# Performance work log

Measured on AMD Instinct MI355X. Metric: run time of the kernel, lower is better.

Reference implementation:

```python
import jax, jax.numpy as jnp
import numpy as np

D = 1024
H = 16
HD = D // H
MLP = 4 * D
EPS = 1e-5


def layernorm(x, g, b):
    mu = jnp.mean(x, axis=-1, keepdims=True)
    var = jnp.mean(jnp.square(x - mu), axis=-1, keepdims=True)
    return (x - mu) * jax.lax.rsqrt(var + EPS) * g + b


def setup_inputs() -> dict:
    key = jax.random.key(0)
    ks = jax.random.split(key, 12)
    s = 0.02
    return {
        "x": jax.random.normal(ks[0], (2, 2048, D), jnp.float32),
        "ln1_g": jnp.ones((D,), jnp.float32),
        "ln1_b": jnp.zeros((D,), jnp.float32),
        "lnm_g": jnp.ones((D,), jnp.float32),
        "lnm_b": jnp.zeros((D,), jnp.float32),
        "qkv_w": jax.random.normal(ks[1], (D, 3 * D), jnp.float32) * s,
        "qkv_b": jnp.zeros((3 * D,), jnp.float32),
        "proj_w": jax.random.normal(ks[2], (D, D), jnp.float32) * s,
        "proj_b": jnp.zeros((D,), jnp.float32),
        "fc1_w": jax.random.normal(ks[3], (D, MLP), jnp.float32) * s,
        "fc1_b": jnp.zeros((MLP,), jnp.float32),
        "fc2_w": jax.random.normal(ks[4], (MLP, D), jnp.float32) * s,
        "fc2_b": jnp.zeros((D,), jnp.float32),
    }


def reference(x, ln1_g, ln1_b, lnm_g, lnm_b, qkv_w, qkv_b, proj_w, proj_b,
              fc1_w, fc1_b, fc2_w, fc2_b):
    B, N, _ = x.shape
    scale = HD ** -0.5
    # --- self-attention on norm1(x) ---
    h = layernorm(x, ln1_g, ln1_b)
    qkv = h @ qkv_w + qkv_b                       # [B, N, 3D]
    qkv = qkv.reshape(B, N, 3, H, HD)
    q, k, v = qkv[:, :, 0], qkv[:, :, 1], qkv[:, :, 2]  # [B, N, H, HD]
    attn = jnp.einsum("bqhd,bkhd->bhqk", q, k) * scale
    attn = jax.nn.softmax(attn, axis=-1)
    o = jnp.einsum("bhqk,bkhd->bqhd", attn, v).reshape(B, N, D)
    x = x + (o @ proj_w + proj_b)
    # --- MLP ---
    m = layernorm(x, lnm_g, lnm_b)
    m = jax.nn.gelu(m @ fc1_w + fc1_b, approximate=False)
    x = x + (m @ fc2_w + fc2_b)
    return x
```

## Files before the change

kernel.cpp:

```cpp
#include <hip/hip_runtime.h>

typedef __bf16 bf16_t;
typedef bf16_t bf16x4 __attribute__((ext_vector_type(4)));
typedef bf16_t bf16x8 __attribute__((ext_vector_type(8)));
typedef float f32x4 __attribute__((ext_vector_type(4)));
typedef unsigned short u16x8 __attribute__((ext_vector_type(8)));

#define MFMA(a, b, c) __builtin_amdgcn_mfma_f32_16x16x32_bf16(a, b, c, 0, 0, 0)

__device__ inline float exp2_fast(float x) {
  float r;
  asm volatile("v_exp_f32 %0, %1" : "=v"(r) : "v"(x));
  return r;
}

__device__ inline void gll16(const bf16_t* g, bf16_t* l) {
  __builtin_amdgcn_global_load_lds(
      (const __attribute__((address_space(1))) unsigned int*)(g),
      (__attribute__((address_space(3))) unsigned int*)(l), 16, 0, 0);
}

__device__ inline float gelu_f(float v) {
  float ax = fabsf(v) * 0.70710678118f;
  float t = __builtin_amdgcn_rcpf(1.0f + 0.3275911f * ax);
  float p = ((((1.061405429f * t - 1.453152027f) * t + 1.421413741f) * t -
              0.284496736f) * t + 0.254829592f) * t;
  float e = exp2_fast(-ax * ax * 1.4426950408889634f);
  float erf = 1.0f - p * e;
  erf = v < 0.f ? -erf : erf;
  return 0.5f * v * (1.0f + erf);
}

__global__ __launch_bounds__(256) void ln_kernel(const float* __restrict__ x,
                                                 const float* __restrict__ g,
                                                 const float* __restrict__ b,
                                                 bf16_t* __restrict__ out) {
  long row = blockIdx.x;
  const float4* xr = (const float4*)(x + row * 1024);
  float4 v = xr[threadIdx.x];
  float s = v.x + v.y + v.z + v.w;
  float s2 = v.x * v.x + v.y * v.y + v.z * v.z + v.w * v.w;
#pragma unroll
  for (int m = 32; m >= 1; m >>= 1) {
    s += __shfl_xor(s, m);
    s2 += __shfl_xor(s2, m);
  }
  __shared__ float red[8];
  int wid = threadIdx.x >> 6;
  if ((threadIdx.x & 63) == 0) {
    red[wid] = s;
    red[4 + wid] = s2;
  }
  __syncthreads();
  s = red[0] + red[1] + red[2] + red[3];
  s2 = red[4] + red[5] + red[6] + red[7];
  float mu = s * (1.f / 1024.f);
  float rs = rsqrtf(s2 * (1.f / 1024.f) - mu * mu + 1e-5f);
  float4 gv = ((const float4*)g)[threadIdx.x];
  float4 bv = ((const float4*)b)[threadIdx.x];
  bf16_t o0 = (bf16_t)((v.x - mu) * rs * gv.x + bv.x);
  bf16_t o1 = (bf16_t)((v.y - mu) * rs * gv.y + bv.y);
  bf16_t o2 = (bf16_t)((v.z - mu) * rs * gv.z + bv.z);
  bf16_t o3 = (bf16_t)((v.w - mu) * rs * gv.w + bv.w);
  ushort4 pk;
  pk.x = *(unsigned short*)&o0;
  pk.y = *(unsigned short*)&o1;
  pk.z = *(unsigned short*)&o2;
  pk.w = *(unsigned short*)&o3;
  *(ushort4*)(out + row * 1024 + threadIdx.x * 4) = pk;
}

__global__ void wconv_kernel(const float* __restrict__ W, bf16_t* __restrict__ Wt,
                             int K, int N) {
  __shared__ float t[32][33];
  int n0 = blockIdx.x * 32, k0 = blockIdx.y * 32;
#pragma unroll
  for (int s = 0; s < 4; s++) {
    int k = threadIdx.y + s * 8;
    t[k][threadIdx.x] = W[(long)(k0 + k) * N + n0 + threadIdx.x];
  }
  __syncthreads();
#pragma unroll
  for (int s = 0; s < 4; s++) {
    int n = threadIdx.y + s * 8;
    Wt[(long)(n0 + n) * K + k0 + threadIdx.x] = (bf16_t)t[threadIdx.x][n];
  }
}

#define STAGE_PTR(DA, DB, k0)                \
  gll16(ga + (k0), DA + w * 1024);           \
  gll16(ga + (k0) + rowstep, DA + w * 1024 + 512); \
  gll16(gb + (k0), DB + w * 1024);           \
  gll16(gb + (k0) + rowstep, DB + w * 1024 + 512);

#define COMPUTE(LA, LB)                                                \
  {                                                                    \
    bf16x8 af[4], bfr[4];                                              \
    _Pragma("unroll") for (int mt = 0; mt < 4; mt++) af[mt] =          \
        *(const bf16x8*)(LA + (wm + mt * 16 + l15) * 32 + quad * 8);   \
    _Pragma("unroll") for (int nt = 0; nt < 4; nt++) bfr[nt] =         \
        *(const bf16x8*)(LB + (wn + nt * 16 + l15) * 32 + quad * 8);   \
    _Pragma("unroll") for (int mt = 0; mt < 4; mt++)                   \
        _Pragma("unroll") for (int nt = 0; nt < 4; nt++) acc[mt][nt] = \
            MFMA(af[mt], bfr[nt], acc[mt][nt]);                        \
  }

#define WB4 asm volatile("s_waitcnt vmcnt(4)\ns_barrier" ::: "memory")
#define WB0 asm volatile("s_waitcnt vmcnt(0)\ns_barrier" ::: "memory")

__global__ __launch_bounds__(256) void gemm_kernel(
    const bf16_t* __restrict__ A, const bf16_t* __restrict__ Bt,
    const float* __restrict__ bias, const float* __restrict__ resid,
    void* __restrict__ Cout, int M, int N, int K, int epi) {
  __shared__ bf16_t lA0[128 * 32], lB0[128 * 32];
  __shared__ bf16_t lA1[128 * 32], lB1[128 * 32];
  __shared__ bf16_t lA2[128 * 32], lB2[128 * 32];
  int tid = threadIdx.x;
  int bn = blockIdx.x, bm = blockIdx.y;
  int kchunk = K / gridDim.z;
  int kbeg = blockIdx.z * kchunk, kend = kbeg + kchunk;

  int lane = tid & 63, w = tid >> 6;
  int quad = lane >> 4, l15 = lane & 15;
  int wm = (w & 1) * 64, wn = (w >> 1) * 64;

  f32x4 acc[4][4];
#pragma unroll
  for (int i = 0; i < 4; i++)
#pragma unroll
    for (int j = 0; j < 4; j++) acc[i][j] = (f32x4){0.f, 0.f, 0.f, 0.f};

  const bf16_t* ga = A + (long)(bm * 128 + w * 32 + (lane >> 2)) * K + (lane & 3) * 8;
  const bf16_t* gb = Bt + (long)(bn * 128 + w * 32 + (lane >> 2)) * K + (lane & 3) * 8;
  long rowstep = (long)16 * K;

  int nit = (kend - kbeg) >> 5;
  bf16_t *A0 = lA0, *A1 = lA1, *A2 = lA2;
  bf16_t *B0 = lB0, *B1 = lB1, *B2 = lB2;
  STAGE_PTR(A0, B0, kbeg);
  STAGE_PTR(A1, B1, kbeg + 32);
  for (int i = 0; i < nit; i++) {
    if (i + 1 < nit) { WB4; } else { WB0; }
    if (i + 2 < nit) {
      int ks = kbeg + (i + 2) * 32;
      STAGE_PTR(A2, B2, ks);
    }
    COMPUTE(A0, B0);
    bf16_t* t;
    t = A0; A0 = A1; A1 = A2; A2 = t;
    t = B0; B0 = B1; B1 = B2; B2 = t;
  }

#pragma unroll
  for (int mt = 0; mt < 4; mt++) {
#pragma unroll
    for (int r = 0; r < 4; r++) {
      long row = bm * 128 + wm + mt * 16 + quad * 4 + r;
#pragma unroll
      for (int nt = 0; nt < 4; nt++) {
        int col = bn * 128 + wn + nt * 16 + l15;
        long idx = row * N + col;
        if (epi == 3) {
          ((bf16_t*)Cout)[(long)blockIdx.z * M * N + idx] = (bf16_t)acc[mt][nt][r];
        } else {
          float v = acc[mt][nt][r] + bias[col];
          if (epi == 1) {
            ((float*)Cout)[idx] = v + resid[idx];
          } else if (epi == 2) {
            ((bf16_t*)Cout)[idx] = (bf16_t)gelu_f(v);
          } else {
            ((bf16_t*)Cout)[idx] = (bf16_t)v;
          }
        }
      }
    }
  }
}

__global__ __launch_bounds__(256) void reduce_ln_kernel(
    const bf16_t* __restrict__ p0, const bf16_t* __restrict__ p1,
    const float* __restrict__ bias, const float* __restrict__ resid,
    float* __restrict__ x1, const float* __restrict__ g,
    const float* __restrict__ bb, bf16_t* __restrict__ mb) {
  long row = blockIdx.x;
  int t = threadIdx.x;
  bf16x4 a = *(const bf16x4*)(p0 + row * 1024 + t * 4);
  bf16x4 c = *(const bf16x4*)(p1 + row * 1024 + t * 4);
  float4 r = ((const float4*)(resid + row * 1024))[t];
  float4 bv = ((const float4*)bias)[t];
  float4 v;
  v.x = (float)a[0] + (float)c[0] + r.x + bv.x;
  v.y = (float)a[1] + (float)c[1] + r.y + bv.y;
  v.z = (float)a[2] + (float)c[2] + r.z + bv.z;
  v.w = (float)a[3] + (float)c[3] + r.w + bv.w;
  ((float4*)(x1 + row * 1024))[t] = v;
  float s = v.x + v.y + v.z + v.w;
  float s2 = v.x * v.x + v.y * v.y + v.z * v.z + v.w * v.w;
#pragma unroll
  for (int m = 32; m >= 1; m >>= 1) {
    s += __shfl_xor(s, m);
    s2 += __shfl_xor(s2, m);
  }
  __shared__ float red[8];
  int wid = t >> 6;
  if ((t & 63) == 0) {
    red[wid] = s;
    red[4 + wid] = s2;
  }
  __syncthreads();
  s = red[0] + red[1] + red[2] + red[3];
  s2 = red[4] + red[5] + red[6] + red[7];
  float mu = s * (1.f / 1024.f);
  float rs = rsqrtf(s2 * (1.f / 1024.f) - mu * mu + 1e-5f);
  float4 gv = ((const float4*)g)[t];
  float4 b2 = ((const float4*)bb)[t];
  bf16_t o0 = (bf16_t)((v.x - mu) * rs * gv.x + b2.x);
  bf16_t o1 = (bf16_t)((v.y - mu) * rs * gv.y + b2.y);
  bf16_t o2 = (bf16_t)((v.z - mu) * rs * gv.z + b2.z);
  bf16_t o3 = (bf16_t)((v.w - mu) * rs * gv.w + b2.w);
  ushort4 pk;
  pk.x = *(unsigned short*)&o0;
  pk.y = *(unsigned short*)&o1;
  pk.z = *(unsigned short*)&o2;
  pk.w = *(unsigned short*)&o3;
  *(ushort4*)(mb + row * 1024 + t * 4) = pk;
}

__global__ __launch_bounds__(256) void reduce4_kernel(const bf16_t* __restrict__ p,
                                                      const float* __restrict__ bias,
                                                      const float* __restrict__ resid,
                                                      float* __restrict__ out) {
  long i = (long)blockIdx.x * 256 + threadIdx.x;
  const long MN = (long)4096 * 1024;
  bf16x4 a0 = *(const bf16x4*)(p + i * 4);
  bf16x4 a1 = *(const bf16x4*)(p + MN + i * 4);
  bf16x4 a2 = *(const bf16x4*)(p + 2 * MN + i * 4);
  bf16x4 a3 = *(const bf16x4*)(p + 3 * MN + i * 4);
  float4 r = ((const float4*)resid)[i];
  float4 bv = ((const float4*)bias)[i & 255];
  float4 o;
  o.x = (float)a0[0] + (float)a1[0] + (float)a2[0] + (float)a3[0] + r.x + bv.x;
  o.y = (float)a0[1] + (float)a1[1] + (float)a2[1] + (float)a3[1] + r.y + bv.y;
  o.z = (float)a0[2] + (float)a1[2] + (float)a2[2] + (float)a3[2] + r.z + bv.z;
  o.w = (float)a0[3] + (float)a1[3] + (float)a2[3] + (float)a3[3] + r.w + bv.w;
  ((float4*)out)[i] = o;
}

#define LDV 72

__global__ __launch_bounds__(256) void attn_kernel(const bf16_t* __restrict__ qkv,
                                                   bf16_t* __restrict__ o) {
  const int LD = 3072;
  int flat = blockIdx.x;
  int slot = flat >> 3;
  int bh = (flat & 7) * 4 + (slot >> 5);
  int qt = slot & 31;
  int h = bh & 15, b = bh >> 4;

  int tid = threadIdx.x, w = tid >> 6, lane = tid & 63;
  int quad = lane >> 4, l15 = lane & 15;
  int qrow = qt * 64 + w * 16;
  const bf16_t* base = qkv + (long)b * 2048 * LD + h * 64;
  const bf16_t* Qp = base;
  const bf16_t* Kp = base + 1024;
  const bf16_t* Vp = base + 2048;

  __shared__ bf16_t lK[2][64 * 64];
  __shared__ bf16_t lV[2][64 * LDV];
  __shared__ bf16_t lP[4][16 * LDV];
  bf16_t* myp = lP[w];

  const bf16_t* kg =
      Kp + (long)(w * 16 + (lane >> 3)) * LD + (((lane & 7) ^ (lane >> 3)) & 7) * 8;
  int kk = tid & 31;
  int d0 = (tid >> 5) * 8;
  const bf16_t* vg = Vp + (long)(2 * kk) * LD + d0;

  gll16(kg, lK[0] + w * 1024);
  gll16(kg + 8 * (long)LD, lK[0] + w * 1024 + 512);
  u16x8 va = *(const u16x8*)(vg);
  u16x8 vb = *(const u16x8*)(vg + LD);
  bf16x8 qf[2];
#pragma unroll
  for (int d = 0; d < 2; d++)
    qf[d] = *(const bf16x8*)(Qp + (long)(qrow + l15) * LD + d * 32 + quad * 8);

  f32x4 oacc[4];
#pragma unroll
  for (int t = 0; t < 4; t++) oacc[t] = (f32x4){0.f, 0.f, 0.f, 0.f};
  float li_p[4] = {0.f, 0.f, 0.f, 0.f};
  const float c2 = 0.18033688011112042f;

  int sw0 = (quad ^ l15) & 7;
  int sw1 = ((quad + 4) ^ l15) & 7;

  for (int it = 0; it < 32; it++) {
    int cur = it & 1, nxt = cur ^ 1;
    asm volatile("s_waitcnt vmcnt(0)\ns_barrier" ::: "memory");
    unsigned int* lvw = (unsigned int*)lV[cur];
#pragma unroll
    for (int j = 0; j < 8; j++)
      lvw[(d0 + j) * (LDV / 2) + kk] = (unsigned int)va[j] | ((unsigned int)vb[j] << 16);
    u16x8 va_n = va, vb_n = vb;
    if (it + 1 < 32) {
      long koff2 = (long)(it + 1) * 64 * LD;
      gll16(kg + koff2, lK[nxt] + w * 1024);
      gll16(kg + koff2 + 8 * (long)LD, lK[nxt] + w * 1024 + 512);
      va_n = *(const u16x8*)(vg + koff2);
      vb_n = *(const u16x8*)(vg + koff2 + LD);
    }
    asm volatile("s_waitcnt lgkmcnt(0)\ns_barrier" ::: "memory");

    f32x4 s[4];
#pragma unroll
    for (int st = 0; st < 4; st++) {
      const bf16_t* krow = lK[cur] + (st * 16 + l15) * 64;
      f32x4 z = (f32x4){0.f, 0.f, 0.f, 0.f};
      z = MFMA(qf[0], *(const bf16x8*)(krow + sw0 * 8), z);
      s[st] = MFMA(qf[1], *(const bf16x8*)(krow + sw1 * 8), z);
    }

#pragma unroll
    for (int st = 0; st < 4; st++)
#pragma unroll
      for (int r = 0; r < 4; r++) {
        float p = exp2_fast(s[st][r] * c2);
        s[st][r] = p;
        li_p[r] += p;
      }

#pragma unroll
    for (int r = 0; r < 4; r++)
#pragma unroll
      for (int st = 0; st < 4; st++)
        myp[(quad * 4 + r) * LDV + st * 16 + l15] = (bf16_t)s[st][r];
    asm volatile("s_waitcnt lgkmcnt(0)" ::: "memory");

    bf16x8 pa0 = *(const bf16x8*)(myp + l15 * LDV + quad * 8);
    bf16x8 pa1 = *(const bf16x8*)(myp + l15 * LDV + 32 + quad * 8);
#pragma unroll
    for (int t = 0; t < 4; t++) {
      const bf16_t* vr = lV[cur] + (t * 16 + l15) * LDV + quad * 8;
      oacc[t] = MFMA(pa0, *(const bf16x8*)(vr), oacc[t]);
      oacc[t] = MFMA(pa1, *(const bf16x8*)(vr + 32), oacc[t]);
    }
    va = va_n;
    vb = vb_n;
  }

  float li[4];
#pragma unroll
  for (int r = 0; r < 4; r++) {
    float s = li_p[r];
#pragma unroll
    for (int x = 8; x >= 1; x >>= 1) s += __shfl_xor(s, x);
    li[r] = s;
  }
#pragma unroll
  for (int t = 0; t < 4; t++)
#pragma unroll
    for (int r = 0; r < 4; r++) {
      long q = qrow + quad * 4 + r;
      o[((long)b * 2048 + q) * 1024 + h * 64 + t * 16 + l15] =
          (bf16_t)(oacc[t][r] / li[r]);
    }
}

extern "C" void kernel_launch(void* const* d_in, const int* in_sizes, int n_in,
                              void* d_out, int out_size, void* d_ws, size_t ws_size,
                              hipStream_t stream) {
  (void)in_sizes; (void)n_in; (void)out_size; (void)ws_size;
  const float* x = (const float*)d_in[0];
  const float* ln1_g = (const float*)d_in[1];
  const float* ln1_b = (const float*)d_in[2];
  const float* lnm_g = (const float*)d_in[3];
  const float* lnm_b = (const float*)d_in[4];
  const float* qkv_w = (const float*)d_in[5];
  const float* qkv_b = (const float*)d_in[6];
  const float* proj_w = (const float*)d_in[7];
  const float* proj_b = (const float*)d_in[8];
  const float* fc1_w = (const float*)d_in[9];
  const float* fc1_b = (const float*)d_in[10];
  const float* fc2_w = (const float*)d_in[11];
  const float* fc2_b = (const float*)d_in[12];
  float* out = (float*)d_out;

  const int M = 4096;
  const int D_ = 1024, MLP_ = 4096, QKV = 3072;

  char* ws = (char*)d_ws;
  bf16_t* h = (bf16_t*)(ws);
  bf16_t* qkvb = (bf16_t*)(ws + (8u << 20));
  bf16_t* ob = (bf16_t*)(ws + (32u << 20));
  float* x1 = (float*)(ws + (40u << 20));
  bf16_t* mb = (bf16_t*)(ws + (56u << 20));
  bf16_t* gb = (bf16_t*)(ws + (64u << 20));
  bf16_t* qkv_wt = (bf16_t*)(ws + (96u << 20));
  bf16_t* proj_wt = (bf16_t*)(ws + (102u << 20));
  bf16_t* fc1_wt = (bf16_t*)(ws + (104u << 20));
  bf16_t* fc2_wt = (bf16_t*)(ws + (112u << 20));
  bf16_t* p_proj = (bf16_t*)(ws + (8u << 20));
  bf16_t* p_fc2 = (bf16_t*)(ws);

  dim3 tb(32, 8);
  wconv_kernel<<<dim3(QKV / 32, D_ / 32), tb, 0, stream>>>(qkv_w, qkv_wt, D_, QKV);
  wconv_kernel<<<dim3(D_ / 32, D_ / 32), tb, 0, stream>>>(proj_w, proj_wt, D_, D_);
  wconv_kernel<<<dim3(MLP_ / 32, D_ / 32), tb, 0, stream>>>(fc1_w, fc1_wt, D_, MLP_);
  wconv_kernel<<<dim3(D_ / 32, MLP_ / 32), tb, 0, stream>>>(fc2_w, fc2_wt, MLP_, D_);

  ln_kernel<<<M, 256, 0, stream>>>(x, ln1_g, ln1_b, h);
  gemm_kernel<<<dim3(QKV / 128, M / 128), 256, 0, stream>>>(h, qkv_wt, qkv_b, nullptr,
                                                            qkvb, M, QKV, D_, 0);
  attn_kernel<<<1024, 256, 0, stream>>>(qkvb, ob);
  gemm_kernel<<<dim3(D_ / 128, M / 128, 2), 256, 0, stream>>>(ob, proj_wt, nullptr,
                                                              nullptr, p_proj, M, D_,
                                                              D_, 3);
  reduce_ln_kernel<<<M, 256, 0, stream>>>(p_proj, p_proj + (long)M * D_, proj_b, x,
                                          x1, lnm_g, lnm_b, mb);
  gemm_kernel<<<dim3(MLP_ / 128, M / 128), 256, 0, stream>>>(mb, fc1_wt, fc1_b, nullptr,
                                                             gb, M, MLP_, D_, 2);
  gemm_kernel<<<dim3(D_ / 128, M / 128, 4), 256, 0, stream>>>(gb, fc2_wt, nullptr,
                                                              nullptr, p_fc2, M, D_,
                                                              MLP_, 3);
  reduce4_kernel<<<4096, 256, 0, stream>>>(p_fc2, fc2_b, x1, out);
}
```

Before: 454.8 us.

## Enlarge GEMM tiles to 256x128 with 512 threads, simplify attention K/V loading

The GEMM kernel moves from 128x128 tiles with 4 waves to 256x128 tiles with 8 waves. The B tile is shared across twice as many rows, which cuts B traffic per output and halves the grid in M. The projection GEMM now uses split-K of 4 instead of 2, so the reduce+LN kernel sums four partials. The attention kernel drops its double-buffered K/V prefetch for a single buffer with synchronous loads and two __syncthreads per tile, which frees LDS but exposes load latency.

```diff
diff --git a/kernel.cpp b/kernel.cpp
--- a/kernel.cpp
+++ b/kernel.cpp
@@ -87,11 +87,10 @@
   }
 }
 
-#define STAGE_PTR(DA, DB, k0)                \
-  gll16(ga + (k0), DA + w * 1024);           \
-  gll16(ga + (k0) + rowstep, DA + w * 1024 + 512); \
-  gll16(gb + (k0), DB + w * 1024);           \
-  gll16(gb + (k0) + rowstep, DB + w * 1024 + 512);
+#define STAGE_PTR(DA, DB, k0)                 \
+  gll16(ga + (k0), DA + w * 512);             \
+  gll16(ga + (k0) + astep, DA + 4096 + w * 512); \
+  gll16(gb + (k0), DB + w * 512);
 
 #define COMPUTE(LA, LB)                                                \
   {                                                                    \
@@ -105,16 +104,16 @@
             MFMA(af[mt], bfr[nt], acc[mt][nt]);                        \
   }
 
-#define WB4 asm volatile("s_waitcnt vmcnt(4)\ns_barrier" ::: "memory")
+#define WB3 asm volatile("s_waitcnt vmcnt(3)\ns_barrier" ::: "memory")
 #define WB0 asm volatile("s_waitcnt vmcnt(0)\ns_barrier" ::: "memory")
 
-__global__ __launch_bounds__(256) void gemm_kernel(
+__global__ __launch_bounds__(512, 4) void gemm_kernel(
     const bf16_t* __restrict__ A, const bf16_t* __restrict__ Bt,
     const float* __restrict__ bias, const float* __restrict__ resid,
     void* __restrict__ Cout, int M, int N, int K, int epi) {
-  __shared__ bf16_t lA0[128 * 32], lB0[128 * 32];
-  __shared__ bf16_t lA1[128 * 32], lB1[128 * 32];
-  __shared__ bf16_t lA2[128 * 32], lB2[128 * 32];
+  __shared__ bf16_t lA0[256 * 32], lB0[128 * 32];
+  __shared__ bf16_t lA1[256 * 32], lB1[128 * 32];
+  __shared__ bf16_t lA2[256 * 32], lB2[128 * 32];
   int tid = threadIdx.x;
   int bn = blockIdx.x, bm = blockIdx.y;
   int kchunk = K / gridDim.z;
@@ -122,7 +121,7 @@
 
   int lane = tid & 63, w = tid >> 6;
   int quad = lane >> 4, l15 = lane & 15;
-  int wm = (w & 1) * 64, wn = (w >> 1) * 64;
+  int wm = (w & 3) * 64, wn = (w >> 2) * 64;
 
   f32x4 acc[4][4];
 #pragma unroll
@@ -130,9 +129,9 @@
 #pragma unroll
     for (int j = 0; j < 4; j++) acc[i][j] = (f32x4){0.f, 0.f, 0.f, 0.f};
 
-  const bf16_t* ga = A + (long)(bm * 128 + w * 32 + (lane >> 2)) * K + (lane & 3) * 8;
-  const bf16_t* gb = Bt + (long)(bn * 128 + w * 32 + (lane >> 2)) * K + (lane & 3) * 8;
-  long rowstep = (long)16 * K;
+  const bf16_t* ga = A + (long)(bm * 256 + w * 16 + (lane >> 2)) * K + (lane & 3) * 8;
+  const bf16_t* gb = Bt + (long)(bn * 128 + w * 16 + (lane >> 2)) * K + (lane & 3) * 8;
+  long astep = (long)128 * K;
 
   int nit = (kend - kbeg) >> 5;
   bf16_t *A0 = lA0, *A1 = lA1, *A2 = lA2;
@@ -140,7 +139,7 @@
   STAGE_PTR(A0, B0, kbeg);
   STAGE_PTR(A1, B1, kbeg + 32);
   for (int i = 0; i < nit; i++) {
-    if (i + 1 < nit) { WB4; } else { WB0; }
+    if (i + 1 < nit) { WB3; } else { WB0; }
     if (i + 2 < nit) {
       int ks = kbeg + (i + 2) * 32;
       STAGE_PTR(A2, B2, ks);
@@ -155,7 +154,7 @@
   for (int mt = 0; mt < 4; mt++) {
 #pragma unroll
     for (int r = 0; r < 4; r++) {
-      long row = bm * 128 + wm + mt * 16 + quad * 4 + r;
+      long row = bm * 256 + wm + mt * 16 + quad * 4 + r;
 #pragma unroll
       for (int nt = 0; nt < 4; nt++) {
         int col = bn * 128 + wn + nt * 16 + l15;
@@ -178,21 +177,24 @@
 }
 
 __global__ __launch_bounds__(256) void reduce_ln_kernel(
-    const bf16_t* __restrict__ p0, const bf16_t* __restrict__ p1,
-    const float* __restrict__ bias, const float* __restrict__ resid,
-    float* __restrict__ x1, const float* __restrict__ g,
-    const float* __restrict__ bb, bf16_t* __restrict__ mb) {
+    const bf16_t* __restrict__ p, const float* __restrict__ bias,
+    const float* __restrict__ resid, float* __restrict__ x1,
+    const float* __restrict__ g, const float* __restrict__ bb,
+    bf16_t* __restrict__ mb) {
+  const long MN = (long)4096 * 1024;
   long row = blockIdx.x;
   int t = threadIdx.x;
-  bf16x4 a = *(const bf16x4*)(p0 + row * 1024 + t * 4);
-  bf16x4 c = *(const bf16x4*)(p1 + row * 1024 + t * 4);
+  bf16x4 a0 = *(const bf16x4*)(p + row * 1024 + t * 4);
+  bf16x4 a1 = *(const bf16x4*)(p + MN + row * 1024 + t * 4);
+  bf16x4 a2 = *(const bf16x4*)(p + 2 * MN + row * 1024 + t * 4);
+  bf16x4 a3 = *(const bf16x4*)(p + 3 * MN + row * 1024 + t * 4);
   float4 r = ((const float4*)(resid + row * 1024))[t];
   float4 bv = ((const float4*)bias)[t];
   float4 v;
-  v.x = (float)a[0] + (float)c[0] + r.x + bv.x;
-  v.y = (float)a[1] + (float)c[1] + r.y + bv.y;
-  v.z = (float)a[2] + (float)c[2] + r.z + bv.z;
-  v.w = (float)a[3] + (float)c[3] + r.w + bv.w;
+  v.x = (float)a0[0] + (float)a1[0] + (float)a2[0] + (float)a3[0] + r.x + bv.x;
+  v.y = (float)a0[1] + (float)a1[1] + (float)a2[1] + (float)a3[1] + r.y + bv.y;
+  v.z = (float)a0[2] + (float)a1[2] + (float)a2[2] + (float)a3[2] + r.z + bv.z;
+  v.w = (float)a0[3] + (float)a1[3] + (float)a2[3] + (float)a3[3] + r.w + bv.w;
   ((float4*)(x1 + row * 1024))[t] = v;
   float s = v.x + v.y + v.z + v.w;
   float s2 = v.x * v.x + v.y * v.y + v.z * v.z + v.w * v.w;
@@ -265,21 +267,19 @@
   const bf16_t* Kp = base + 1024;
   const bf16_t* Vp = base + 2048;
 
-  __shared__ bf16_t lK[2][64 * 64];
-  __shared__ bf16_t lV[2][64 * LDV];
+  __shared__ bf16_t lK[64 * 64];
+  __shared__ bf16_t lV[64 * LDV];
   __shared__ bf16_t lP[4][16 * LDV];
   bf16_t* myp = lP[w];
 
   const bf16_t* kg =
       Kp + (long)(w * 16 + (lane >> 3)) * LD + (((lane & 7) ^ (lane >> 3)) & 7) * 8;
+  bf16_t* lkd = lK + w * 1024;
   int kk = tid & 31;
   int d0 = (tid >> 5) * 8;
   const bf16_t* vg = Vp + (long)(2 * kk) * LD + d0;
-
-  gll16(kg, lK[0] + w * 1024);
-  gll16(kg + 8 * (long)LD, lK[0] + w * 1024 + 512);
-  u16x8 va = *(const u16x8*)(vg);
-  u16x8 vb = *(const u16x8*)(vg + LD);
+  unsigned int* lvw = (unsigned int*)lV;
+
   bf16x8 qf[2];
 #pragma unroll
   for (int d = 0; d < 2; d++)
@@ -294,27 +294,22 @@
   int sw0 = (quad ^ l15) & 7;
   int sw1 = ((quad + 4) ^ l15) & 7;
 
-  for (int it = 0; it < 32; it++) {
-    int cur = it & 1, nxt = cur ^ 1;
-    asm volatile("s_waitcnt vmcnt(0)\ns_barrier" ::: "memory");
-    unsigned int* lvw = (unsigned int*)lV[cur];
+  for (int kt = 0; kt < 2048; kt += 64) {
+    long koff = (long)kt * LD;
+    u16x8 va = *(const u16x8*)(vg + koff);
+    u16x8 vb = *(const u16x8*)(vg + koff + LD);
+    __syncthreads();
+    gll16(kg + koff, lkd);
+    gll16(kg + koff + 8 * (long)LD, lkd + 512);
 #pragma unroll
     for (int j = 0; j < 8; j++)
       lvw[(d0 + j) * (LDV / 2) + kk] = (unsigned int)va[j] | ((unsigned int)vb[j] << 16);
-    u16x8 va_n = va, vb_n = vb;
-    if (it + 1 < 32) {
-      long koff2 = (long)(it + 1) * 64 * LD;
-      gll16(kg + koff2, lK[nxt] + w * 1024);
-      gll16(kg + koff2 + 8 * (long)LD, lK[nxt] + w * 1024 + 512);
-      va_n = *(const u16x8*)(vg + koff2);
-      vb_n = *(const u16x8*)(vg + koff2 + LD);
-    }
-    asm volatile("s_waitcnt lgkmcnt(0)\ns_barrier" ::: "memory");
+    __syncthreads();
 
     f32x4 s[4];
 #pragma unroll
     for (int st = 0; st < 4; st++) {
-      const bf16_t* krow = lK[cur] + (st * 16 + l15) * 64;
+      const bf16_t* krow = lK + (st * 16 + l15) * 64;
       f32x4 z = (f32x4){0.f, 0.f, 0.f, 0.f};
       z = MFMA(qf[0], *(const bf16x8*)(krow + sw0 * 8), z);
       s[st] = MFMA(qf[1], *(const bf16x8*)(krow + sw1 * 8), z);
@@ -340,12 +335,10 @@
     bf16x8 pa1 = *(const bf16x8*)(myp + l15 * LDV + 32 + quad * 8);
 #pragma unroll
     for (int t = 0; t < 4; t++) {
-      const bf16_t* vr = lV[cur] + (t * 16 + l15) * LDV + quad * 8;
+      const bf16_t* vr = lV + (t * 16 + l15) * LDV + quad * 8;
       oacc[t] = MFMA(pa0, *(const bf16x8*)(vr), oacc[t]);
       oacc[t] = MFMA(pa1, *(const bf16x8*)(vr + 32), oacc[t]);
     }
-    va = va_n;
-    vb = vb_n;
   }
 
   float li[4];
@@ -399,7 +392,7 @@
   bf16_t* proj_wt = (bf16_t*)(ws + (102u << 20));
   bf16_t* fc1_wt = (bf16_t*)(ws + (104u << 20));
   bf16_t* fc2_wt = (bf16_t*)(ws + (112u << 20));
-  bf16_t* p_proj = (bf16_t*)(ws + (8u << 20));
+  bf16_t* p_proj = (bf16_t*)(ws);
   bf16_t* p_fc2 = (bf16_t*)(ws);
 
   dim3 tb(32, 8);
@@ -409,17 +402,17 @@
   wconv_kernel<<<dim3(D_ / 32, MLP_ / 32), tb, 0, stream>>>(fc2_w, fc2_wt, MLP_, D_);
 
   ln_kernel<<<M, 256, 0, stream>>>(x, ln1_g, ln1_b, h);
-  gemm_kernel<<<dim3(QKV / 128, M / 128), 256, 0, stream>>>(h, qkv_wt, qkv_b, nullptr,
+  gemm_kernel<<<dim3(QKV / 128, M / 256), 512, 0, stream>>>(h, qkv_wt, qkv_b, nullptr,
                                                             qkvb, M, QKV, D_, 0);
   attn_kernel<<<1024, 256, 0, stream>>>(qkvb, ob);
-  gemm_kernel<<<dim3(D_ / 128, M / 128, 2), 256, 0, stream>>>(ob, proj_wt, nullptr,
+  gemm_kernel<<<dim3(D_ / 128, M / 256, 4), 512, 0, stream>>>(ob, proj_wt, nullptr,
                                                               nullptr, p_proj, M, D_,
                                                               D_, 3);
-  reduce_ln_kernel<<<M, 256, 0, stream>>>(p_proj, p_proj + (long)M * D_, proj_b, x,
-                                          x1, lnm_g, lnm_b, mb);
-  gemm_kernel<<<dim3(MLP_ / 128, M / 128), 256, 0, stream>>>(mb, fc1_wt, fc1_b, nullptr,
-                                                             gb, M, MLP_, D_, 2);
-  gemm_kernel<<<dim3(D_ / 128, M / 128, 4), 256, 0, stream>>>(gb, fc2_wt, nullptr,
+  reduce_ln_kernel<<<M, 256, 0, stream>>>(p_proj, proj_b, x, x1, lnm_g, lnm_b, mb);
+  gemm_kernel<<<dim3(MLP_ / 128, M / 256), 512, 0, stream>>>(mb, fc1_wt, fc1_b,
+                                                             nullptr, gb, M, MLP_, D_,
+                                                             2);
+  gemm_kernel<<<dim3(D_ / 128, M / 256, 4), 512, 0, stream>>>(gb, fc2_wt, nullptr,
                                                               nullptr, p_fc2, M, D_,
                                                               MLP_, 3);
   reduce4_kernel<<<4096, 256, 0, stream>>>(p_fc2, fc2_b, x1, out);
```

New measurement: 405.1 us. -10.9%, faster.
